# Optimization experiments

Hardware: AMD Instinct MI355X
Metric: run time of the kernel (lower is better)

The kernel has to match this reference:

```python
import jax, jax.numpy as jnp
import numpy as np

N, M, D = 32768, 4096, 128  # samples, SOM units (64x64), input_dim
GRID_H, GRID_W = 64, 64


def setup_inputs() -> dict:
    key = jax.random.key(0)
    k1, k2 = jax.random.split(key)
    inputs = jax.random.normal(k1, (N, D), dtype=jnp.float32)
    # SOM2D.__init__: weights = torch.rand(size, input_dim)
    weights = jax.random.uniform(k2, (M, D), dtype=jnp.float32)
    # grid = meshgrid(arange(H), arange(W)) -> [M, 2] integer unit coordinates
    gx, gy = jnp.meshgrid(jnp.arange(GRID_H), jnp.arange(GRID_W), indexing='ij')
    grid = jnp.stack([gx, gy], axis=-1).reshape(-1, 2).astype(jnp.int32)
    return {"inputs": inputs, "weights": weights, "grid": grid}


def reference(inputs, weights, grid):
    # sed(x, y): squared Euclidean distance [N, M].
    # tensor the torch code materializes; same math.
    x_sq = jnp.sum(inputs * inputs, axis=1, keepdims=True)        # [N, 1]
    w_sq = jnp.sum(weights * weights, axis=1)                      # [M]
    cross = jnp.einsum('nd,md->nm', inputs, weights)               # [N, M]
    distances = x_sq + w_sq - 2.0 * cross                          # [N, M]
    # wtac: argmin over units, then lookup grid coordinates of the winner.
    winning_indices = jnp.argmin(distances, axis=1)                # [N]
    winning_labels = grid[winning_indices]                         # [N, 2]
    return winning_labels
```

## Files before the change

### kernel.cpp

```cpp
#include <hip/hip_runtime.h>
#include <float.h>
#include <stdint.h>


constexpr int D = 128;

typedef _Float16 f16x8 __attribute__((ext_vector_type(8)));
typedef float    f32x4 __attribute__((ext_vector_type(4)));

__global__ void wsq_kernel(const float* __restrict__ w, float* __restrict__ wsq, int M) {
    int u = blockIdx.x * blockDim.x + threadIdx.x;
    if (u >= M) return;
    const float4* wp = reinterpret_cast<const float4*>(w + (size_t)u * D);
    float a0 = 0.f, a1 = 0.f, a2 = 0.f, a3 = 0.f;
#pragma unroll
    for (int k = 0; k < D / 4; ++k) {
        float4 v = wp[k];
        a0 = fmaf(v.x, v.x, a0); a1 = fmaf(v.y, v.y, a1);
        a2 = fmaf(v.z, v.z, a2); a3 = fmaf(v.w, v.w, a3);
    }
    wsq[u] = (a0 + a1) + (a2 + a3);
}

__global__ void keys_init(unsigned long long* __restrict__ keys, int N) {
    int i = blockIdx.x * blockDim.x + threadIdx.x;
    if (i < N) keys[i] = ~0ull;
}

__global__ void finalize(const unsigned long long* __restrict__ keys,
                         const int* __restrict__ grid, int* __restrict__ out, int N) {
    int s = blockIdx.x * blockDim.x + threadIdx.x;
    if (s >= N) return;
    int idx = (int)(unsigned)(keys[s] & 0xFFFFFFFFull);
    out[2 * s]     = grid[2 * idx];
    out[2 * s + 1] = grid[2 * idx + 1];
}

__device__ __forceinline__ void cvt_split(const float4& a0, const float4& a1,
                                          f16x8& h, f16x8& l) {
    float v[8] = {a0.x, a0.y, a0.z, a0.w, a1.x, a1.y, a1.z, a1.w};
#pragma unroll
    for (int j = 0; j < 8; ++j) {
        _Float16 hh = (_Float16)v[j];
        h[j] = hh;
        l[j] = (_Float16)(v[j] - (float)hh);
    }
}

template <bool ATOMIC>
__global__ __launch_bounds__(256, 2) void som_mfma(
        const float* __restrict__ x, const float* __restrict__ w,
        const float* __restrict__ wsq, const int* __restrict__ grid,
        int* __restrict__ out, unsigned long long* __restrict__ keys,
        int unitGroups, int M) {
    __shared__ f16x8 hbuf[1024];
    __shared__ f16x8 lbuf[1024];

    const int tid  = threadIdx.x;
    const int lane = tid & 63;
    const int wv   = tid >> 6;
    const int c    = lane & 15;
    const int q    = lane >> 4;

    const int ug       = blockIdx.x % unitGroups;
    const int sg       = blockIdx.x / unitGroups;
    const int sBase    = sg * 256 + wv * 64;
    const int unitsPer = M / unitGroups;
    const int uStart   = ug * unitsPer;
    const int nTiles   = unitsPer / 64;

    f16x8 Ah[16], Al[16];
#pragma unroll
    for (int i = 0; i < 4; ++i) {
        const float* xr = x + (size_t)(sBase + 16 * i + c) * D + q * 8;
#pragma unroll
        for (int s = 0; s < 4; ++s) {
            float4 a0 = *reinterpret_cast<const float4*>(xr + 32 * s);
            float4 a1 = *reinterpret_cast<const float4*>(xr + 32 * s + 4);
            cvt_split(a0, a1, Ah[i * 4 + s], Al[i * 4 + s]);
        }
    }

    float bestD[16];
    int   bestI[16];
#pragma unroll
    for (int sl = 0; sl < 16; ++sl) { bestD[sl] = FLT_MAX; bestI[sl] = 0; }

    for (int tile = 0; tile < nTiles; ++tile) {
        const int uTile = uStart + tile * 64;
        __syncthreads();
#pragma unroll
        for (int it = 0; it < 4; ++it) {
            int p   = tid + 256 * it;
            int row = p & 63;
            int cp  = p >> 6;
            const float* wp = w + (size_t)(uTile + row) * D + cp * 8;
            float4 b0 = *reinterpret_cast<const float4*>(wp);
            float4 b1 = *reinterpret_cast<const float4*>(wp + 4);
            f16x8 h, l;
            cvt_split(b0, b1, h, l);
            int slot = ((cp >> 2) * 4 + (row >> 4)) * 64 + (cp & 3) * 16 + (row & 15);
            hbuf[slot] = h;
            lbuf[slot] = l;
        }
        __syncthreads();

        f32x4 acc[16];
#pragma unroll
        for (int f = 0; f < 16; ++f) acc[f] = (f32x4){0.f, 0.f, 0.f, 0.f};

#pragma unroll
        for (int s = 0; s < 4; ++s) {
            f16x8 bf[4];
#pragma unroll
            for (int t = 0; t < 4; ++t) bf[t] = hbuf[(s * 4 + t) * 64 + lane];
#pragma unroll
            for (int i = 0; i < 4; ++i)
#pragma unroll
                for (int t = 0; t < 4; ++t)
                    acc[i * 4 + t] = __builtin_amdgcn_mfma_f32_16x16x32_f16(
                        Ah[i * 4 + s], bf[t], acc[i * 4 + t], 0, 0, 0);
#pragma unroll
            for (int i = 0; i < 4; ++i)
#pragma unroll
                for (int t = 0; t < 4; ++t)
                    acc[i * 4 + t] = __builtin_amdgcn_mfma_f32_16x16x32_f16(
                        Al[i * 4 + s], bf[t], acc[i * 4 + t], 0, 0, 0);
#pragma unroll
            for (int t = 0; t < 4; ++t) bf[t] = lbuf[(s * 4 + t) * 64 + lane];
#pragma unroll
            for (int i = 0; i < 4; ++i)
#pragma unroll
                for (int t = 0; t < 4; ++t)
                    acc[i * 4 + t] = __builtin_amdgcn_mfma_f32_16x16x32_f16(
                        Ah[i * 4 + s], bf[t], acc[i * 4 + t], 0, 0, 0);
        }

#pragma unroll
        for (int t = 0; t < 4; ++t) {
            const int n   = uTile + 16 * t + c;
            const float wq = wsq[n];
#pragma unroll
            for (int i = 0; i < 4; ++i) {
                f32x4 a = acc[i * 4 + t];
#pragma unroll
                for (int r = 0; r < 4; ++r) {
                    float score = fmaf(-2.f, a[r], wq);
                    int sl = i * 4 + r;
                    if (score < bestD[sl]) { bestD[sl] = score; bestI[sl] = n; }
                }
            }
        }
    }

#pragma unroll
    for (int sl = 0; sl < 16; ++sl) {
        float d   = bestD[sl];
        int   idx = bestI[sl];
#pragma unroll
        for (int m = 1; m < 16; m <<= 1) {
            float od = __shfl_xor(d, m, 64);
            int   oi = __shfl_xor(idx, m, 64);
            if (od < d || (od == d && oi < idx)) { d = od; idx = oi; }
        }
        if (c == 0) {
            const int sOut = sBase + 16 * (sl >> 2) + 4 * q + (sl & 3);
            if (ATOMIC) {
                unsigned ub = __float_as_uint(d);
                ub = (ub & 0x80000000u) ? ~ub : (ub | 0x80000000u);
                unsigned long long key = ((unsigned long long)ub << 32) | (unsigned)idx;
                atomicMin(&keys[sOut], key);
            } else {
                out[2 * sOut]     = grid[2 * idx];
                out[2 * sOut + 1] = grid[2 * idx + 1];
            }
        }
    }
}

extern "C" void kernel_launch(void* const* d_in, const int* in_sizes, int n_in,
                              void* d_out, int out_size, void* d_ws, size_t ws_size,
                              hipStream_t stream) {
    const float* x    = (const float*)d_in[0];
    const float* w    = (const float*)d_in[1];
    const int*   grid = (const int*)d_in[2];
    int* out = (int*)d_out;

    const int N = in_sizes[0] / D;
    const int M = in_sizes[1] / D;

    const size_t keysBytes = (size_t)N * 8;
    const bool bigWs = ws_size >= keysBytes + (size_t)M * 4;

    if (bigWs) {
        unsigned long long* keys = (unsigned long long*)d_ws;
        float* wsq = (float*)((char*)d_ws + keysBytes);
        keys_init<<<(N + 255) / 256, 256, 0, stream>>>(keys, N);
        wsq_kernel<<<(M + 255) / 256, 256, 0, stream>>>(w, wsq, M);
        const int UG = 4;
        som_mfma<true><<<(N / 256) * UG, 256, 0, stream>>>(
            x, w, wsq, grid, out, keys, UG, M);
        finalize<<<(N + 255) / 256, 256, 0, stream>>>(keys, grid, out, N);
    } else {
        float* wsq = (float*)d_ws;
        wsq_kernel<<<(M + 255) / 256, 256, 0, stream>>>(w, wsq, M);
        som_mfma<false><<<N / 256, 256, 0, stream>>>(
            x, w, wsq, grid, out, nullptr, 1, M);
    }
}
```

Before: 191.0 us.

## Precompute split-fp16 weight tiles globally and stream them without LDS staging

Adds a prep kernel that converts weights once into hi/lo fp16 fragments in MFMA-ready tile layout and fuses the ||w||^2 computation. The main kernel reads these fragments straight from global memory (L2), which removes per-block conversion, LDS staging and __syncthreads. Each wave now covers 32 samples instead of 64, and the unit split drops from 4 groups to 2. Atomics are replaced by per-group partial keys that finalize reduces, which also removes keys_init. In exchange, weight-fragment reuse per load is halved and each tile is fetched from global memory with no LDS sharing across waves.

```diff
diff --git a/kernel.cpp b/kernel.cpp
--- a/kernel.cpp
+++ b/kernel.cpp
@@ -8,71 +8,74 @@
 typedef _Float16 f16x8 __attribute__((ext_vector_type(8)));
 typedef float    f32x4 __attribute__((ext_vector_type(4)));
 
-__global__ void wsq_kernel(const float* __restrict__ w, float* __restrict__ wsq, int M) {
-    int u = blockIdx.x * blockDim.x + threadIdx.x;
-    if (u >= M) return;
-    const float4* wp = reinterpret_cast<const float4*>(w + (size_t)u * D);
-    float a0 = 0.f, a1 = 0.f, a2 = 0.f, a3 = 0.f;
-#pragma unroll
-    for (int k = 0; k < D / 4; ++k) {
-        float4 v = wp[k];
-        a0 = fmaf(v.x, v.x, a0); a1 = fmaf(v.y, v.y, a1);
-        a2 = fmaf(v.z, v.z, a2); a3 = fmaf(v.w, v.w, a3);
-    }
-    wsq[u] = (a0 + a1) + (a2 + a3);
-}
-
-__global__ void keys_init(unsigned long long* __restrict__ keys, int N) {
-    int i = blockIdx.x * blockDim.x + threadIdx.x;
-    if (i < N) keys[i] = ~0ull;
+__device__ __forceinline__ void cvt_split(const float4& a0, const float4& a1,
+                                          f16x8& h, f16x8& l) {
+    float v[8] = {a0.x, a0.y, a0.z, a0.w, a1.x, a1.y, a1.z, a1.w};
+#pragma unroll
+    for (int j = 0; j < 8; ++j) {
+        _Float16 hh = (_Float16)v[j];
+        h[j] = hh;
+        l[j] = (_Float16)(v[j] - (float)hh);
+    }
+}
+
+__global__ __launch_bounds__(256) void prep_kernel(
+        const float* __restrict__ w, f16x8* __restrict__ hG,
+        f16x8* __restrict__ lG, float* __restrict__ wsq, int M) {
+    int g = blockIdx.x * 256 + threadIdx.x;
+    if (g >= M * 16) return;
+    int u = g >> 4, o = g & 15;
+    const float4* wp = reinterpret_cast<const float4*>(w + (size_t)u * D + o * 8);
+    float4 a0 = wp[0], a1 = wp[1];
+    f16x8 h, l;
+    cvt_split(a0, a1, h, l);
+    float ss = 0.f;
+    ss = fmaf(a0.x, a0.x, ss); ss = fmaf(a0.y, a0.y, ss);
+    ss = fmaf(a0.z, a0.z, ss); ss = fmaf(a0.w, a0.w, ss);
+    ss = fmaf(a1.x, a1.x, ss); ss = fmaf(a1.y, a1.y, ss);
+    ss = fmaf(a1.z, a1.z, ss); ss = fmaf(a1.w, a1.w, ss);
+#pragma unroll
+    for (int m = 1; m < 16; m <<= 1) ss += __shfl_xor(ss, m, 64);
+    if (o == 0) wsq[u] = ss;
+    int slot = (((u >> 6) * 16 + (o >> 2) * 4 + ((u >> 4) & 3)) << 6)
+             + ((o & 3) << 4) + (u & 15);
+    hG[slot] = h;
+    lG[slot] = l;
 }
 
 __global__ void finalize(const unsigned long long* __restrict__ keys,
                          const int* __restrict__ grid, int* __restrict__ out, int N) {
     int s = blockIdx.x * blockDim.x + threadIdx.x;
     if (s >= N) return;
-    int idx = (int)(unsigned)(keys[s] & 0xFFFFFFFFull);
+    unsigned long long k0 = keys[s];
+    unsigned long long k1 = keys[(size_t)N + s];
+    unsigned long long k = k1 < k0 ? k1 : k0;
+    int idx = (int)(unsigned)(k & 0xFFFFFFFFull);
     out[2 * s]     = grid[2 * idx];
     out[2 * s + 1] = grid[2 * idx + 1];
 }
 
-__device__ __forceinline__ void cvt_split(const float4& a0, const float4& a1,
-                                          f16x8& h, f16x8& l) {
-    float v[8] = {a0.x, a0.y, a0.z, a0.w, a1.x, a1.y, a1.z, a1.w};
-#pragma unroll
-    for (int j = 0; j < 8; ++j) {
-        _Float16 hh = (_Float16)v[j];
-        h[j] = hh;
-        l[j] = (_Float16)(v[j] - (float)hh);
-    }
-}
-
-template <bool ATOMIC>
-__global__ __launch_bounds__(256, 2) void som_mfma(
-        const float* __restrict__ x, const float* __restrict__ w,
-        const float* __restrict__ wsq, const int* __restrict__ grid,
-        int* __restrict__ out, unsigned long long* __restrict__ keys,
-        int unitGroups, int M) {
-    __shared__ f16x8 hbuf[1024];
-    __shared__ f16x8 lbuf[1024];
-
+template <bool PARTIAL>
+__global__ __launch_bounds__(256, 2) void som_main(
+        const float* __restrict__ x, const f16x8* __restrict__ hG,
+        const f16x8* __restrict__ lG, const float* __restrict__ wsq,
+        const int* __restrict__ grid, int* __restrict__ out,
+        unsigned long long* __restrict__ keys,
+        int unitGroups, int M, int N) {
     const int tid  = threadIdx.x;
     const int lane = tid & 63;
     const int wv   = tid >> 6;
     const int c    = lane & 15;
     const int q    = lane >> 4;
 
-    const int ug       = blockIdx.x % unitGroups;
-    const int sg       = blockIdx.x / unitGroups;
-    const int sBase    = sg * 256 + wv * 64;
-    const int unitsPer = M / unitGroups;
-    const int uStart   = ug * unitsPer;
-    const int nTiles   = unitsPer / 64;
-
-    f16x8 Ah[16], Al[16];
-#pragma unroll
-    for (int i = 0; i < 4; ++i) {
-        const float* xr = x + (size_t)(sBase + 16 * i + c) * D + q * 8;
+    const int ug    = blockIdx.x % unitGroups;
+    const int sg    = blockIdx.x / unitGroups;
+    const int sWave = sg * 128 + wv * 32;
+
+    f16x8 Ah[8], Al[8];
+#pragma unroll
+    for (int i = 0; i < 2; ++i) {
+        const float* xr = x + (size_t)(sWave + 16 * i + c) * D + q * 8;
 #pragma unroll
         for (int s = 0; s < 4; ++s) {
             float4 a0 = *reinterpret_cast<const float4*>(xr + 32 * s);
@@ -81,67 +84,58 @@
         }
     }
 
-    float bestD[16];
-    int   bestI[16];
-#pragma unroll
-    for (int sl = 0; sl < 16; ++sl) { bestD[sl] = FLT_MAX; bestI[sl] = 0; }
-
-    for (int tile = 0; tile < nTiles; ++tile) {
-        const int uTile = uStart + tile * 64;
-        __syncthreads();
-#pragma unroll
-        for (int it = 0; it < 4; ++it) {
-            int p   = tid + 256 * it;
-            int row = p & 63;
-            int cp  = p >> 6;
-            const float* wp = w + (size_t)(uTile + row) * D + cp * 8;
-            float4 b0 = *reinterpret_cast<const float4*>(wp);
-            float4 b1 = *reinterpret_cast<const float4*>(wp + 4);
-            f16x8 h, l;
-            cvt_split(b0, b1, h, l);
-            int slot = ((cp >> 2) * 4 + (row >> 4)) * 64 + (cp & 3) * 16 + (row & 15);
-            hbuf[slot] = h;
-            lbuf[slot] = l;
-        }
-        __syncthreads();
-
-        f32x4 acc[16];
-#pragma unroll
-        for (int f = 0; f < 16; ++f) acc[f] = (f32x4){0.f, 0.f, 0.f, 0.f};
+    float bestD[8];
+    int   bestI[8];
+#pragma unroll
+    for (int sl = 0; sl < 8; ++sl) { bestD[sl] = FLT_MAX; bestI[sl] = 0; }
+
+    const int tilesPer = (M / 64) / unitGroups;
+    const int tile0    = ug * tilesPer;
+
+    for (int tt = 0; tt < tilesPer; ++tt) {
+        const int tile = tile0 + tt;
+        const f16x8* hp = hG + ((size_t)tile << 10) + lane;
+        const f16x8* lp = lG + ((size_t)tile << 10) + lane;
+
+        f32x4 acc[8];
+#pragma unroll
+        for (int f = 0; f < 8; ++f) acc[f] = (f32x4){0.f, 0.f, 0.f, 0.f};
 
 #pragma unroll
         for (int s = 0; s < 4; ++s) {
-            f16x8 bf[4];
-#pragma unroll
-            for (int t = 0; t < 4; ++t) bf[t] = hbuf[(s * 4 + t) * 64 + lane];
-#pragma unroll
-            for (int i = 0; i < 4; ++i)
+            f16x8 bh[4], bl[4];
+#pragma unroll
+            for (int t = 0; t < 4; ++t) {
+                bh[t] = hp[(size_t)(s * 4 + t) << 6];
+                bl[t] = lp[(size_t)(s * 4 + t) << 6];
+            }
+#pragma unroll
+            for (int i = 0; i < 2; ++i)
 #pragma unroll
                 for (int t = 0; t < 4; ++t)
                     acc[i * 4 + t] = __builtin_amdgcn_mfma_f32_16x16x32_f16(
-                        Ah[i * 4 + s], bf[t], acc[i * 4 + t], 0, 0, 0);
-#pragma unroll
-            for (int i = 0; i < 4; ++i)
+                        Ah[i * 4 + s], bh[t], acc[i * 4 + t], 0, 0, 0);
+#pragma unroll
+            for (int i = 0; i < 2; ++i)
 #pragma unroll
                 for (int t = 0; t < 4; ++t)
                     acc[i * 4 + t] = __builtin_amdgcn_mfma_f32_16x16x32_f16(
-                        Al[i * 4 + s], bf[t], acc[i * 4 + t], 0, 0, 0);
-#pragma unroll
-            for (int t = 0; t < 4; ++t) bf[t] = lbuf[(s * 4 + t) * 64 + lane];
-#pragma unroll
-            for (int i = 0; i < 4; ++i)
+                        Al[i * 4 + s], bh[t], acc[i * 4 + t], 0, 0, 0);
+#pragma unroll
+            for (int i = 0; i < 2; ++i)
 #pragma unroll
                 for (int t = 0; t < 4; ++t)
                     acc[i * 4 + t] = __builtin_amdgcn_mfma_f32_16x16x32_f16(
-                        Ah[i * 4 + s], bf[t], acc[i * 4 + t], 0, 0, 0);
-        }
-
+                        Ah[i * 4 + s], bl[t], acc[i * 4 + t], 0, 0, 0);
+        }
+
+        const int uTile = tile * 64;
 #pragma unroll
         for (int t = 0; t < 4; ++t) {
-            const int n   = uTile + 16 * t + c;
+            const int n    = uTile + 16 * t + c;
             const float wq = wsq[n];
 #pragma unroll
-            for (int i = 0; i < 4; ++i) {
+            for (int i = 0; i < 2; ++i) {
                 f32x4 a = acc[i * 4 + t];
 #pragma unroll
                 for (int r = 0; r < 4; ++r) {
@@ -154,7 +148,7 @@
     }
 
 #pragma unroll
-    for (int sl = 0; sl < 16; ++sl) {
+    for (int sl = 0; sl < 8; ++sl) {
         float d   = bestD[sl];
         int   idx = bestI[sl];
 #pragma unroll
@@ -164,12 +158,12 @@
             if (od < d || (od == d && oi < idx)) { d = od; idx = oi; }
         }
         if (c == 0) {
-            const int sOut = sBase + 16 * (sl >> 2) + 4 * q + (sl & 3);
-            if (ATOMIC) {
+            const int sOut = sWave + 16 * (sl >> 2) + 4 * q + (sl & 3);
+            if (PARTIAL) {
                 unsigned ub = __float_as_uint(d);
                 ub = (ub & 0x80000000u) ? ~ub : (ub | 0x80000000u);
                 unsigned long long key = ((unsigned long long)ub << 32) | (unsigned)idx;
-                atomicMin(&keys[sOut], key);
+                keys[(size_t)ug * N + sOut] = key;
             } else {
                 out[2 * sOut]     = grid[2 * idx];
                 out[2 * sOut + 1] = grid[2 * idx + 1];
@@ -189,22 +183,25 @@
     const int N = in_sizes[0] / D;
     const int M = in_sizes[1] / D;
 
-    const size_t keysBytes = (size_t)N * 8;
-    const bool bigWs = ws_size >= keysBytes + (size_t)M * 4;
-
-    if (bigWs) {
-        unsigned long long* keys = (unsigned long long*)d_ws;
-        float* wsq = (float*)((char*)d_ws + keysBytes);
-        keys_init<<<(N + 255) / 256, 256, 0, stream>>>(keys, N);
-        wsq_kernel<<<(M + 255) / 256, 256, 0, stream>>>(w, wsq, M);
-        const int UG = 4;
-        som_mfma<true><<<(N / 256) * UG, 256, 0, stream>>>(
-            x, w, wsq, grid, out, keys, UG, M);
+    const size_t hlBytes   = (size_t)M * D * 2;
+    const size_t baseBytes = 2 * hlBytes + (size_t)M * 4;
+    const size_t keysBytes = 2 * (size_t)N * 8;
+
+    f16x8* hG  = (f16x8*)d_ws;
+    f16x8* lG  = (f16x8*)((char*)d_ws + hlBytes);
+    float* wsq = (float*)((char*)d_ws + 2 * hlBytes);
+    unsigned long long* keys = (unsigned long long*)((char*)d_ws + baseBytes);
+
+    prep_kernel<<<(M * 16 + 255) / 256, 256, 0, stream>>>(w, hG, lG, wsq, M);
+
+    const int sampleGroups = N / 128;
+    if (ws_size >= baseBytes + keysBytes) {
+        const int UG = 2;
+        som_main<true><<<sampleGroups * UG, 256, 0, stream>>>(
+            x, hG, lG, wsq, grid, out, keys, UG, M, N);
         finalize<<<(N + 255) / 256, 256, 0, stream>>>(keys, grid, out, N);
     } else {
-        float* wsq = (float*)d_ws;
-        wsq_kernel<<<(M + 255) / 256, 256, 0, stream>>>(w, wsq, M);
-        som_mfma<false><<<N / 256, 256, 0, stream>>>(
-            x, w, wsq, grid, out, nullptr, 1, M);
-    }
-}
+        som_main<false><<<sampleGroups, 256, 0, stream>>>(
+            x, hG, lG, wsq, grid, out, nullptr, 1, M, N);
+    }
+}
```

Result: slower. 195.3 us (+2.3%).
